# Kernel optimization log

Measured on AMD Instinct MI355X. Metric: run time of the kernel, lower is better.

Reference implementation:

```python
import jax, jax.numpy as jnp
import numpy as np

LAMBD = 0.2   # model.lambd
T_MAX = 1000  # model.T
TOL = 1e-10


def _softshrink(v, lam):
    return jnp.sign(v) * jnp.maximum(jnp.abs(v) - lam, 0.0)


def setup_inputs() -> dict:
    key = jax.random.key(0)
    k1, k2, k3 = jax.random.split(key, 3)
    n, m, N = 64, 256, 1024
    D = jax.random.normal(k1, (n, m), dtype=jnp.float32)
    D = D / jnp.linalg.norm(D, axis=0)                      # unit-norm atoms
    w = jax.random.normal(k2, (m,), dtype=jnp.float32)
    w = w / jnp.linalg.norm(w)
    x = jax.random.normal(k3, (N, n), dtype=jnp.float32)
    x = x / jnp.linalg.norm(x, axis=1, keepdims=True)       # unit-norm samples (as in generate_data)
    return {"x": x, "D": D, "w": w}


def _encode(x_t, D, lambd):
    # x_t: (n, N), D: (n, m). Faithful to encode(): ISTA with detached D/x,
    # then per-sample least-squares refinement on the support (vectorized as
    # a masked batched solve instead of a python loop over samples).
    m = D.shape[1]
    Dg = jax.lax.stop_gradient(D)
    xg = jax.lax.stop_gradient(x_t)
    # eta = 1/||D||_2^2 is a constant in torch (computed from numpy at init)
    eta = jax.lax.stop_gradient(1.0 / jnp.linalg.norm(Dg, ord=2) ** 2)
    thr = lambd * eta

    z0 = _softshrink(eta * (Dg.T @ xg), thr)                # (m, N)

    def cond(c):
        i, _, diff = c
        return (i < T_MAX) & (diff >= TOL)

    def body(c):
        i, z, _ = c
        res = Dg @ z - xg                                   # (n, N)
        znew = _softshrink(z - eta * (Dg.T @ res), thr)     # (m, N)
        return (i + 1, znew, jnp.linalg.norm(znew - z))

    _, z, _ = jax.lax.while_loop(
        cond, body, (jnp.int32(0), z0, jnp.array(jnp.inf, dtype=x_t.dtype))
    )
    z = jax.lax.stop_gradient(z)                            # ISTA output is fully detached in torch

    # Support refinement: alfa[S,i] = inv(D_S^T D_S) (D_S^T x_i - lambd*signs_S)
    mask = z != 0                                           # (m, N) support sets
    signs = jnp.sign(z)                                     # constant (sign has zero grad)
    M = mask.T.astype(x_t.dtype)                            # (N, m)
    G = D.T @ D                                             # (m, m) Gram (with grad, model.D)
    b = M * (x_t.T @ D - lambd * signs.T)                   # (N, m), zero off-support
    # Masked Gram: identity on off-support rows/cols -> block solve equals submatrix solve
    A = M[:, :, None] * M[:, None, :] * G[None] \
        + jnp.eye(m, dtype=x_t.dtype) * (1.0 - M)[:, :, None]   # (N, m, m)
    solved = jnp.linalg.solve(A, b[..., None])[..., 0]      # (N, m)
    alfa = jnp.where(mask, solved.T, z)                     # (m, N)
    return alfa


def reference(x, D, w):
    # x: (N, n). forward(): z = encode(x); y = w @ z; pred = [y, -y]
    z = _encode(x.T, D, LAMBD)                              # (m, N)
    y = w @ z                                               # (N,)
    return jnp.stack([y, -y], axis=1)                       # (N, 2)
```

## Files before the change

### kernel.cpp

```cpp
#include <hip/hip_runtime.h>

#define LAMBD 0.2f
#define KMAX 128
#define KS 64
#define OS 1.9f

using half8 = __attribute__((ext_vector_type(8))) _Float16;
using f32x4 = __attribute__((ext_vector_type(4))) float;

__device__ __forceinline__ float sshrink(float v, float thr) {
    float c = fminf(fmaxf(v, -thr), thr);
    return v - c;
}

__device__ __forceinline__ unsigned pack2(_Float16 a, _Float16 b) {
    unsigned short ua = __builtin_bit_cast(unsigned short, a);
    unsigned short ub = __builtin_bit_cast(unsigned short, b);
    return (unsigned)ua | ((unsigned)ub << 16);
}

__global__ __launch_bounds__(256) void prep_all(const float* __restrict__ xg,
                                                const float* __restrict__ Dg,
                                                float* __restrict__ ws,
                                                float* __restrict__ Gfull,
                                                float* __restrict__ cbuf)
{
    const int t = threadIdx.x;
    if (blockIdx.x == 0) {
        __shared__ __align__(16) float Dc[256 * 68];
        __shared__ __align__(16) float Bm[64 * 68];
        __shared__ float vv[64];
        __shared__ float part[4 * 64];
        __shared__ float lamsh;

        for (int i = 0; i < 64; ++i)
            Dc[t * 68 + i] = Dg[i * 256 + t];
        __syncthreads();

        const int ti = t >> 4, tj = t & 15;
        float acc[4][4];
        #pragma unroll
        for (int r = 0; r < 4; ++r)
            #pragma unroll
            for (int c = 0; c < 4; ++c) acc[r][c] = 0.f;
        for (int mm = 0; mm < 256; ++mm) {
            const float4 A = *(const float4*)&Dc[mm * 68 + 4 * ti];
            const float4 Bv = *(const float4*)&Dc[mm * 68 + 4 * tj];
            const float Ae[4] = {A.x, A.y, A.z, A.w};
            const float Be[4] = {Bv.x, Bv.y, Bv.z, Bv.w};
            #pragma unroll
            for (int r = 0; r < 4; ++r)
                #pragma unroll
                for (int c = 0; c < 4; ++c)
                    acc[r][c] += Ae[r] * Be[c];
        }
        #pragma unroll
        for (int r = 0; r < 4; ++r)
            #pragma unroll
            for (int c = 0; c < 4; ++c)
                Bm[(4 * ti + r) * 68 + (4 * tj + c)] = acc[r][c];
        if (t < 64) vv[t] = 0.125f;
        __syncthreads();

        for (int itp = 0; itp < 64; ++itp) {
            const int p = t >> 6, i = t & 63;
            float partial = 0.f;
            #pragma unroll
            for (int jj = 0; jj < 16; ++jj) {
                const int j = p * 16 + jj;
                partial += Bm[j * 68 + i] * vv[j];
            }
            part[p * 64 + i] = partial;
            __syncthreads();
            if (t < 64) {
                float nv = part[t] + part[64 + t] + part[128 + t] + part[192 + t];
                float n2 = nv * nv;
                for (int d = 1; d < 64; d <<= 1) n2 += __shfl_xor(n2, d);
                vv[t] = nv * rsqrtf(n2);
                if (t == 0) lamsh = n2;
            }
            __syncthreads();
        }
        if (t == 0) ws[0] = OS / sqrtf(lamsh);
    } else {
        __shared__ float xsh[4][64];
        const int r = blockIdx.x - 1;
        const int s0 = r * 4;
        xsh[t >> 6][t & 63] = xg[s0 * 64 + t];
        __syncthreads();

        float accG = 0.f, a0 = 0.f, a1 = 0.f, a2 = 0.f, a3 = 0.f;
        #pragma unroll
        for (int i = 0; i < 64; ++i) {
            const float dv = Dg[i * 256 + t];
            const float dr = Dg[i * 256 + r];
            accG += dr * dv;
            a0 += xsh[0][i] * dv;
            a1 += xsh[1][i] * dv;
            a2 += xsh[2][i] * dv;
            a3 += xsh[3][i] * dv;
        }
        Gfull[r * 256 + t] = accG;
        cbuf[(s0 + 0) * 256 + t] = a0;
        cbuf[(s0 + 1) * 256 + t] = a1;
        cbuf[(s0 + 2) * 256 + t] = a2;
        cbuf[(s0 + 3) * 256 + t] = a3;
    }
}

__global__ __launch_bounds__(256, 1) void ista_solve(const float* __restrict__ cbuf,
                                                     const float* __restrict__ Gfull,
                                                     const float* __restrict__ ws,
                                                     const float* __restrict__ wg,
                                                     float* __restrict__ zbuf,
                                                     int* __restrict__ kflag,
                                                     float* __restrict__ out)
{
    __shared__ __align__(16) _Float16 dbuf[2][16][264];
    __shared__ int chgs[4];
    __shared__ __align__(16) float znb[4][264];
    __shared__ __align__(16) float Gm[4][KS * (KS + 1)];
    __shared__ int   idxs[4][KS];
    __shared__ float sgns[4][KS];

    const int t = threadIdx.x;
    const int w = t >> 6, l = t & 63;
    const int n = l & 15, kg = l >> 4;
    const int s0 = blockIdx.x * 4;
    const float s = ws[0];
    const float thr = LAMBD * s;
    const float S = 1.0f / 2048.0f;
    const float FLUSH = 6.2e-5f;

    half8 wh[4][8], wl[4][8];
    #pragma unroll
    for (int a = 0; a < 4; ++a) {
        const int row = 64 * w + 16 * a + n;
        #pragma unroll
        for (int kt = 0; kt < 8; ++kt) {
            const float4 g0 = *(const float4*)&Gfull[row * 256 + kt * 32 + kg * 8];
            const float4 g1 = *(const float4*)&Gfull[row * 256 + kt * 32 + kg * 8 + 4];
            const float ge[8] = {g0.x, g0.y, g0.z, g0.w, g1.x, g1.y, g1.z, g1.w};
            half8 h, lo;
            #pragma unroll
            for (int j = 0; j < 8; ++j) {
                const int col = kt * 32 + kg * 8 + j;
                const float wv = (row == col ? 1.0f : 0.0f) - s * ge[j];
                const _Float16 whj = (_Float16)wv;
                h[j] = whj;
                lo[j] = (_Float16)((wv - (float)whj) * 2048.0f);
            }
            wh[a][kt] = h;
            wl[a][kt] = lo;
        }
    }

    float bv[4][4], z[4][4], znv[4][4];
    #pragma unroll
    for (int a = 0; a < 4; ++a)
        #pragma unroll
        for (int jj = 0; jj < 4; ++jj) {
            const int row = 64 * w + 16 * a + 4 * kg + jj;
            bv[a][jj] = (n < 4) ? s * cbuf[(s0 + n) * 256 + row] : 0.f;
            z[a][jj] = 0.f;
        }

    f32x4 acc1[4], acc2[4];
    #pragma unroll
    for (int a = 0; a < 4; ++a) {
        acc1[a] = (f32x4){0.f, 0.f, 0.f, 0.f};
        acc2[a] = (f32x4){0.f, 0.f, 0.f, 0.f};
    }

    int cur = 0;
    for (int it = 0; ; ++it) {
        bool anyflag = false;
        _Float16 dh16[4][4];
        #pragma unroll
        for (int a = 0; a < 4; ++a)
            #pragma unroll
            for (int jj = 0; jj < 4; ++jj) {
                const float P = acc1[a][jj] + S * acc2[a][jj];
                const float zn = sshrink(P + bv[a][jj], thr);
                znv[a][jj] = zn;
                const float d = zn - z[a][jj];
                const bool live = fabsf(d) >= FLUSH;
                anyflag |= live;
                const _Float16 hd = live ? (_Float16)d : (_Float16)0.0f;
                dh16[a][jj] = hd;
                z[a][jj] += (float)hd;
            }
        if (it == 1000) break;

        const int anyw = __any(anyflag);
        if (l == 0) chgs[w] = anyw;
        #pragma unroll
        for (int a = 0; a < 4; ++a) {
            const unsigned lo = pack2(dh16[a][0], dh16[a][1]);
            const unsigned hi = pack2(dh16[a][2], dh16[a][3]);
            *(uint2*)&dbuf[cur][n][64 * w + 16 * a + 4 * kg] = make_uint2(lo, hi);
        }
        __syncthreads();
        if (!(chgs[0] | chgs[1] | chgs[2] | chgs[3])) break;

        half8 dh[8];
        #pragma unroll
        for (int kt = 0; kt < 8; ++kt)
            dh[kt] = *(const half8*)&dbuf[cur][n][kt * 32 + kg * 8];

        #pragma unroll
        for (int kt = 0; kt < 8; ++kt)
            #pragma unroll
            for (int a = 0; a < 4; ++a) {
                acc1[a] = __builtin_amdgcn_mfma_f32_16x16x32_f16(wh[a][kt], dh[kt], acc1[a], 0, 0, 0);
                acc2[a] = __builtin_amdgcn_mfma_f32_16x16x32_f16(wl[a][kt], dh[kt], acc2[a], 0, 0, 0);
            }
        cur ^= 1;
    }

    if (n < 4) {
        #pragma unroll
        for (int a = 0; a < 4; ++a) {
            float4 v = make_float4(znv[a][0], znv[a][1], znv[a][2], znv[a][3]);
            *(float4*)&znb[n][64 * w + 16 * a + 4 * kg] = v;
        }
    }
    __syncthreads();

    const int sample = s0 + w;
    const float4 zz = *(const float4*)&znb[w][4 * l];
    const int c0 = zz.x != 0.f, c1 = zz.y != 0.f, c2 = zz.z != 0.f, c3 = zz.w != 0.f;
    const int cnt = c0 + c1 + c2 + c3;
    int scan = cnt;
    for (int d = 1; d < 64; d <<= 1) {
        const int v = __shfl_up(scan, d);
        if (l >= d) scan += v;
    }
    int o = scan - cnt;
    const int k = __shfl(scan, 63);

    if (k == 0) {
        if (l == 0) {
            kflag[sample] = 0;
            out[sample * 2] = 0.f;
            out[sample * 2 + 1] = 0.f;
        }
        return;
    }
    if (k > KS) {
        if (l == 0) kflag[sample] = 1;
        #pragma unroll
        for (int q = 0; q < 4; ++q)
            zbuf[sample * 256 + 4 * l + q] = ((const float*)&zz)[q];
        return;
    }
    if (l == 0) kflag[sample] = 0;

    if (c0) { idxs[w][o] = 4 * l + 0; sgns[w][o] = zz.x > 0.f ? 1.f : -1.f; ++o; }
    if (c1) { idxs[w][o] = 4 * l + 1; sgns[w][o] = zz.y > 0.f ? 1.f : -1.f; ++o; }
    if (c2) { idxs[w][o] = 4 * l + 2; sgns[w][o] = zz.z > 0.f ? 1.f : -1.f; ++o; }
    if (c3) { idxs[w][o] = 4 * l + 3; sgns[w][o] = zz.w > 0.f ? 1.f : -1.f; ++o; }

    const int   ib = idxs[w][(l < k) ? l : (k - 1)];
    const float sg = (l < k) ? sgns[w][l] : 0.f;
    float rhs = (l < k) ? (cbuf[sample * 256 + ib] - LAMBD * sg) : 0.f;

    for (int a = 0; a < k; ++a) {
        const int ra = __shfl(ib, a);
        if (l < k) Gm[w][a * (KS + 1) + l] = Gfull[ra * 256 + ib];
    }

    float dinv = 0.f;
    for (int j = 0; j < k; ++j) {
        const float Gjj = Gm[w][j * (KS + 1) + j];
        const float Ljj = sqrtf(fmaxf(Gjj, 1e-30f));
        const float iv = 1.0f / Ljj;
        float Laj = 0.f;
        if (l == j) { Gm[w][j * (KS + 1) + j] = Ljj; dinv = iv; }
        if (l > j && l < k) { Laj = Gm[w][l * (KS + 1) + j] * iv; Gm[w][l * (KS + 1) + j] = Laj; }
        for (int b = j + 1; b < k; ++b) {
            const float Lbj = Gm[w][b * (KS + 1) + j];
            if (l >= b && l < k) Gm[w][l * (KS + 1) + b] -= Laj * Lbj;
        }
    }

    float y = rhs;
    for (int j = 0; j < k; ++j) {
        const float Laj = Gm[w][l * (KS + 1) + j];
        const float yjf = __shfl(y, j) * __shfl(dinv, j);
        if (l == j) y = yjf;
        if (l > j) y -= Laj * yjf;
    }
    float xv = y;
    for (int j = k - 1; j >= 0; --j) {
        const float Lja = Gm[w][j * (KS + 1) + l];
        const float xjf = __shfl(xv, j) * __shfl(dinv, j);
        if (l == j) xv = xjf;
        if (l < j) xv -= Lja * xjf;
    }

    float acc = (l < k) ? wg[ib] * xv : 0.f;
    for (int d = 1; d < 64; d <<= 1) acc += __shfl_xor(acc, d);
    if (l == 0) { out[sample * 2] = acc; out[sample * 2 + 1] = -acc; }
}

__global__ __launch_bounds__(64) void solve_big(const float* __restrict__ Gfull,
                                                const float* __restrict__ cbuf,
                                                const float* __restrict__ wg,
                                                const float* __restrict__ zbuf,
                                                const int* __restrict__ kflag,
                                                float* __restrict__ out)
{
    __shared__ __align__(16) float Gm[KMAX * (KMAX + 1)];
    __shared__ int   idx[KMAX];
    __shared__ float sgn[KMAX];
    __shared__ float rhs[KMAX];
    __shared__ float sol[KMAX];

    const int l = threadIdx.x;
    const int sample = blockIdx.x;
    if (!kflag[sample]) return;

    const float4 zz = ((const float4*)(zbuf + sample * 256))[l];
    const int c0 = zz.x != 0.f, c1 = zz.y != 0.f, c2 = zz.z != 0.f, c3 = zz.w != 0.f;
    const int cnt = c0 + c1 + c2 + c3;
    int scan = cnt;
    for (int d = 1; d < 64; d <<= 1) {
        const int v = __shfl_up(scan, d);
        if (l >= d) scan += v;
    }
    int o = scan - cnt;
    int k = __shfl(scan, 63);
    if (k > KMAX) k = KMAX;
    if (c0) { if (o < KMAX) { idx[o] = 4 * l + 0; sgn[o] = zz.x > 0.f ? 1.f : -1.f; } ++o; }
    if (c1) { if (o < KMAX) { idx[o] = 4 * l + 1; sgn[o] = zz.y > 0.f ? 1.f : -1.f; } ++o; }
    if (c2) { if (o < KMAX) { idx[o] = 4 * l + 2; sgn[o] = zz.z > 0.f ? 1.f : -1.f; } ++o; }
    if (c3) { if (o < KMAX) { idx[o] = 4 * l + 3; sgn[o] = zz.w > 0.f ? 1.f : -1.f; } ++o; }
    __syncthreads();

    for (int a = 0; a < k; ++a) {
        const int ra = idx[a];
        for (int b = l; b < k; b += 64)
            Gm[a * (KMAX + 1) + b] = Gfull[ra * 256 + idx[b]];
    }
    for (int a = l; a < k; a += 64)
        rhs[a] = cbuf[sample * 256 + idx[a]] - LAMBD * sgn[a];
    __syncthreads();

    for (int j = 0; j < k; ++j) {
        const float Ljj = sqrtf(fmaxf(Gm[j * (KMAX + 1) + j], 1e-30f));
        const float inv = 1.0f / Ljj;
        if (l == 0) Gm[j * (KMAX + 1) + j] = Ljj;
        for (int a = j + 1 + l; a < k; a += 64)
            Gm[a * (KMAX + 1) + j] *= inv;
        __syncthreads();
        for (int b = j + 1; b < k; ++b) {
            const float Lbj = Gm[b * (KMAX + 1) + j];
            for (int a = b + l; a < k; a += 64)
                Gm[a * (KMAX + 1) + b] -= Gm[a * (KMAX + 1) + j] * Lbj;
        }
        __syncthreads();
    }
    for (int j = 0; j < k; ++j) {
        const float yj = rhs[j] / Gm[j * (KMAX + 1) + j];
        if (l == 0) sol[j] = yj;
        for (int a = j + 1 + l; a < k; a += 64)
            rhs[a] -= Gm[a * (KMAX + 1) + j] * yj;
        __syncthreads();
    }
    for (int j = k - 1; j >= 0; --j) {
        const float xj = sol[j] / Gm[j * (KMAX + 1) + j];
        if (l == 0) sol[j] = xj;
        for (int a = l; a < j; a += 64)
            sol[a] -= Gm[j * (KMAX + 1) + a] * xj;
        __syncthreads();
    }
    float acc = 0.f;
    for (int a = l; a < k; a += 64)
        acc += wg[idx[a]] * sol[a];
    for (int d = 1; d < 64; d <<= 1) acc += __shfl_xor(acc, d);
    if (l == 0) { out[sample * 2] = acc; out[sample * 2 + 1] = -acc; }
}

extern "C" void kernel_launch(void* const* d_in, const int* in_sizes, int n_in,
                              void* d_out, int out_size, void* d_ws, size_t ws_size,
                              hipStream_t stream) {
    const float* x = (const float*)d_in[0];
    const float* D = (const float*)d_in[1];
    const float* w = (const float*)d_in[2];
    float* out = (float*)d_out;
    float* ws  = (float*)d_ws;

    float* Gfull = ws + 256;
    float* zbuf  = ws + 256 + 65536;
    float* cbuf  = ws + 256 + 65536 + 262144;
    int*   kflag = (int*)(ws + 256 + 65536 + 262144 + 262144);

    prep_all<<<257, 256, 0, stream>>>(x, D, ws, Gfull, cbuf);
    ista_solve<<<256, 256, 0, stream>>>(cbuf, Gfull, ws, w, zbuf, kflag, out);
    solve_big<<<1024, 64, 0, stream>>>(Gfull, cbuf, w, zbuf, kflag, out);
}
```

Baseline: 243.7 us.

## Switch ISTA to FISTA momentum and fold large-support solve into main kernel

Replaces the over-relaxed ISTA step (1.9/L) with standard 1/L FISTA, adding Nesterov momentum on the iterate and sending deltas of the extrapolated point through the MFMA update. The aim is to reach the convergence tolerance in fewer iterations. The separate solve_big kernel and its zbuf/kflag round trip are removed: supports larger than 64 are now solved inside ista_solve by the whole block, which saves one launch but serializes these solves per block. The power iteration count also drops from 64 to 40. FISTA is not monotone, so it may converge to a different support, and the stop test on small deltas behaves differently under momentum.

```diff
diff --git a/kernel.cpp b/kernel.cpp
--- a/kernel.cpp
+++ b/kernel.cpp
@@ -3,7 +3,6 @@
 #define LAMBD 0.2f
 #define KMAX 128
 #define KS 64
-#define OS 1.9f
 
 using half8 = __attribute__((ext_vector_type(8))) _Float16;
 using f32x4 = __attribute__((ext_vector_type(4))) float;
@@ -62,7 +61,7 @@
         if (t < 64) vv[t] = 0.125f;
         __syncthreads();
 
-        for (int itp = 0; itp < 64; ++itp) {
+        for (int itp = 0; itp < 40; ++itp) {
             const int p = t >> 6, i = t & 63;
             float partial = 0.f;
             #pragma unroll
@@ -81,7 +80,7 @@
             }
             __syncthreads();
         }
-        if (t == 0) ws[0] = OS / sqrtf(lamsh);
+        if (t == 0) ws[0] = 1.0f / sqrtf(lamsh);
     } else {
         __shared__ float xsh[4][64];
         const int r = blockIdx.x - 1;
@@ -112,16 +111,18 @@
                                                      const float* __restrict__ Gfull,
                                                      const float* __restrict__ ws,
                                                      const float* __restrict__ wg,
-                                                     float* __restrict__ zbuf,
-                                                     int* __restrict__ kflag,
                                                      float* __restrict__ out)
 {
     __shared__ __align__(16) _Float16 dbuf[2][16][264];
     __shared__ int chgs[4];
     __shared__ __align__(16) float znb[4][264];
-    __shared__ __align__(16) float Gm[4][KS * (KS + 1)];
-    __shared__ int   idxs[4][KS];
-    __shared__ float sgns[4][KS];
+    __shared__ __align__(16) float GmPool[16640];
+    __shared__ int   idxPool[256];
+    __shared__ float sgnPool[256];
+    __shared__ float rhsF[KMAX];
+    __shared__ float solF[KMAX];
+    __shared__ int   big4[4];
+    __shared__ int   kbig;
 
     const int t = threadIdx.x;
     const int w = t >> 6, l = t & 63;
@@ -155,14 +156,15 @@
         }
     }
 
-    float bv[4][4], z[4][4], znv[4][4];
+    float bv[4][4], y[4][4], zo[4][4], zn[4][4];
     #pragma unroll
     for (int a = 0; a < 4; ++a)
         #pragma unroll
         for (int jj = 0; jj < 4; ++jj) {
             const int row = 64 * w + 16 * a + 4 * kg + jj;
             bv[a][jj] = (n < 4) ? s * cbuf[(s0 + n) * 256 + row] : 0.f;
-            z[a][jj] = 0.f;
+            y[a][jj] = 0.f;
+            zo[a][jj] = 0.f;
         }
 
     f32x4 acc1[4], acc2[4];
@@ -172,8 +174,11 @@
         acc2[a] = (f32x4){0.f, 0.f, 0.f, 0.f};
     }
 
+    float tk = 1.0f;
     int cur = 0;
     for (int it = 0; ; ++it) {
+        const float tk1 = 0.5f * (1.0f + sqrtf(1.0f + 4.0f * tk * tk));
+        const float beta = (tk - 1.0f) / tk1;
         bool anyflag = false;
         _Float16 dh16[4][4];
         #pragma unroll
@@ -181,15 +186,18 @@
             #pragma unroll
             for (int jj = 0; jj < 4; ++jj) {
                 const float P = acc1[a][jj] + S * acc2[a][jj];
-                const float zn = sshrink(P + bv[a][jj], thr);
-                znv[a][jj] = zn;
-                const float d = zn - z[a][jj];
+                const float z = sshrink(P + bv[a][jj], thr);
+                zn[a][jj] = z;
+                const float yn = z + beta * (z - zo[a][jj]);
+                zo[a][jj] = z;
+                const float d = yn - y[a][jj];
                 const bool live = fabsf(d) >= FLUSH;
                 anyflag |= live;
                 const _Float16 hd = live ? (_Float16)d : (_Float16)0.0f;
                 dh16[a][jj] = hd;
-                z[a][jj] += (float)hd;
-            }
+                y[a][jj] += (float)hd;
+            }
+        tk = tk1;
         if (it == 1000) break;
 
         const int anyw = __any(anyflag);
@@ -221,13 +229,17 @@
     if (n < 4) {
         #pragma unroll
         for (int a = 0; a < 4; ++a) {
-            float4 v = make_float4(znv[a][0], znv[a][1], znv[a][2], znv[a][3]);
+            float4 v = make_float4(zn[a][0], zn[a][1], zn[a][2], zn[a][3]);
             *(float4*)&znb[n][64 * w + 16 * a + 4 * kg] = v;
         }
     }
     __syncthreads();
 
     const int sample = s0 + w;
+    float* Gw = GmPool + w * (KS * (KS + 1));
+    int*   idxW = idxPool + w * KS;
+    float* sgnW = sgnPool + w * KS;
+
     const float4 zz = *(const float4*)&znb[w][4 * l];
     const int c0 = zz.x != 0.f, c1 = zz.y != 0.f, c2 = zz.z != 0.f, c3 = zz.w != 0.f;
     const int cnt = c0 + c1 + c2 + c3;
@@ -238,148 +250,140 @@
     }
     int o = scan - cnt;
     const int k = __shfl(scan, 63);
+    if (l == 0) big4[w] = (k > KS) ? 1 : 0;
 
     if (k == 0) {
-        if (l == 0) {
-            kflag[sample] = 0;
-            out[sample * 2] = 0.f;
-            out[sample * 2 + 1] = 0.f;
-        }
-        return;
-    }
-    if (k > KS) {
-        if (l == 0) kflag[sample] = 1;
-        #pragma unroll
-        for (int q = 0; q < 4; ++q)
-            zbuf[sample * 256 + 4 * l + q] = ((const float*)&zz)[q];
-        return;
-    }
-    if (l == 0) kflag[sample] = 0;
-
-    if (c0) { idxs[w][o] = 4 * l + 0; sgns[w][o] = zz.x > 0.f ? 1.f : -1.f; ++o; }
-    if (c1) { idxs[w][o] = 4 * l + 1; sgns[w][o] = zz.y > 0.f ? 1.f : -1.f; ++o; }
-    if (c2) { idxs[w][o] = 4 * l + 2; sgns[w][o] = zz.z > 0.f ? 1.f : -1.f; ++o; }
-    if (c3) { idxs[w][o] = 4 * l + 3; sgns[w][o] = zz.w > 0.f ? 1.f : -1.f; ++o; }
-
-    const int   ib = idxs[w][(l < k) ? l : (k - 1)];
-    const float sg = (l < k) ? sgns[w][l] : 0.f;
-    float rhs = (l < k) ? (cbuf[sample * 256 + ib] - LAMBD * sg) : 0.f;
-
-    for (int a = 0; a < k; ++a) {
-        const int ra = __shfl(ib, a);
-        if (l < k) Gm[w][a * (KS + 1) + l] = Gfull[ra * 256 + ib];
-    }
-
-    float dinv = 0.f;
-    for (int j = 0; j < k; ++j) {
-        const float Gjj = Gm[w][j * (KS + 1) + j];
-        const float Ljj = sqrtf(fmaxf(Gjj, 1e-30f));
-        const float iv = 1.0f / Ljj;
-        float Laj = 0.f;
-        if (l == j) { Gm[w][j * (KS + 1) + j] = Ljj; dinv = iv; }
-        if (l > j && l < k) { Laj = Gm[w][l * (KS + 1) + j] * iv; Gm[w][l * (KS + 1) + j] = Laj; }
-        for (int b = j + 1; b < k; ++b) {
-            const float Lbj = Gm[w][b * (KS + 1) + j];
-            if (l >= b && l < k) Gm[w][l * (KS + 1) + b] -= Laj * Lbj;
-        }
-    }
-
-    float y = rhs;
-    for (int j = 0; j < k; ++j) {
-        const float Laj = Gm[w][l * (KS + 1) + j];
-        const float yjf = __shfl(y, j) * __shfl(dinv, j);
-        if (l == j) y = yjf;
-        if (l > j) y -= Laj * yjf;
-    }
-    float xv = y;
-    for (int j = k - 1; j >= 0; --j) {
-        const float Lja = Gm[w][j * (KS + 1) + l];
-        const float xjf = __shfl(xv, j) * __shfl(dinv, j);
-        if (l == j) xv = xjf;
-        if (l < j) xv -= Lja * xjf;
-    }
-
-    float acc = (l < k) ? wg[ib] * xv : 0.f;
-    for (int d = 1; d < 64; d <<= 1) acc += __shfl_xor(acc, d);
-    if (l == 0) { out[sample * 2] = acc; out[sample * 2 + 1] = -acc; }
-}
-
-__global__ __launch_bounds__(64) void solve_big(const float* __restrict__ Gfull,
-                                                const float* __restrict__ cbuf,
-                                                const float* __restrict__ wg,
-                                                const float* __restrict__ zbuf,
-                                                const int* __restrict__ kflag,
-                                                float* __restrict__ out)
-{
-    __shared__ __align__(16) float Gm[KMAX * (KMAX + 1)];
-    __shared__ int   idx[KMAX];
-    __shared__ float sgn[KMAX];
-    __shared__ float rhs[KMAX];
-    __shared__ float sol[KMAX];
-
-    const int l = threadIdx.x;
-    const int sample = blockIdx.x;
-    if (!kflag[sample]) return;
-
-    const float4 zz = ((const float4*)(zbuf + sample * 256))[l];
-    const int c0 = zz.x != 0.f, c1 = zz.y != 0.f, c2 = zz.z != 0.f, c3 = zz.w != 0.f;
-    const int cnt = c0 + c1 + c2 + c3;
-    int scan = cnt;
-    for (int d = 1; d < 64; d <<= 1) {
-        const int v = __shfl_up(scan, d);
-        if (l >= d) scan += v;
-    }
-    int o = scan - cnt;
-    int k = __shfl(scan, 63);
-    if (k > KMAX) k = KMAX;
-    if (c0) { if (o < KMAX) { idx[o] = 4 * l + 0; sgn[o] = zz.x > 0.f ? 1.f : -1.f; } ++o; }
-    if (c1) { if (o < KMAX) { idx[o] = 4 * l + 1; sgn[o] = zz.y > 0.f ? 1.f : -1.f; } ++o; }
-    if (c2) { if (o < KMAX) { idx[o] = 4 * l + 2; sgn[o] = zz.z > 0.f ? 1.f : -1.f; } ++o; }
-    if (c3) { if (o < KMAX) { idx[o] = 4 * l + 3; sgn[o] = zz.w > 0.f ? 1.f : -1.f; } ++o; }
+        if (l == 0) { out[sample * 2] = 0.f; out[sample * 2 + 1] = 0.f; }
+    } else if (k <= KS) {
+        if (c0) { idxW[o] = 4 * l + 0; sgnW[o] = zz.x > 0.f ? 1.f : -1.f; ++o; }
+        if (c1) { idxW[o] = 4 * l + 1; sgnW[o] = zz.y > 0.f ? 1.f : -1.f; ++o; }
+        if (c2) { idxW[o] = 4 * l + 2; sgnW[o] = zz.z > 0.f ? 1.f : -1.f; ++o; }
+        if (c3) { idxW[o] = 4 * l + 3; sgnW[o] = zz.w > 0.f ? 1.f : -1.f; ++o; }
+        __builtin_amdgcn_wave_barrier();
+
+        const int   ib = idxW[(l < k) ? l : (k - 1)];
+        const float sg = (l < k) ? sgnW[l] : 0.f;
+        float rhs = (l < k) ? (cbuf[sample * 256 + ib] - LAMBD * sg) : 0.f;
+
+        for (int a = 0; a < k; ++a) {
+            const int ra = __shfl(ib, a);
+            if (l < k) Gw[a * (KS + 1) + l] = Gfull[ra * 256 + ib];
+        }
+        __builtin_amdgcn_wave_barrier();
+
+        float dinv = 0.f;
+        for (int j = 0; j < k; ++j) {
+            const float Gjj = Gw[j * (KS + 1) + j];
+            const float Ljj = sqrtf(fmaxf(Gjj, 1e-30f));
+            const float iv = 1.0f / Ljj;
+            float Laj = 0.f;
+            if (l == j) { Gw[j * (KS + 1) + j] = Ljj; dinv = iv; }
+            if (l > j && l < k) { Laj = Gw[l * (KS + 1) + j] * iv; Gw[l * (KS + 1) + j] = Laj; }
+            __builtin_amdgcn_wave_barrier();
+            for (int b = j + 1; b < k; ++b) {
+                const float Lbj = Gw[b * (KS + 1) + j];
+                if (l >= b && l < k) Gw[l * (KS + 1) + b] -= Laj * Lbj;
+            }
+            __builtin_amdgcn_wave_barrier();
+        }
+
+        float yv = rhs;
+        for (int j = 0; j < k; ++j) {
+            const float Laj = Gw[l * (KS + 1) + j];
+            const float yjf = __shfl(yv, j) * __shfl(dinv, j);
+            if (l == j) yv = yjf;
+            if (l > j) yv -= Laj * yjf;
+        }
+        float xv = yv;
+        for (int j = k - 1; j >= 0; --j) {
+            const float Lja = Gw[j * (KS + 1) + l];
+            const float xjf = __shfl(xv, j) * __shfl(dinv, j);
+            if (l == j) xv = xjf;
+            if (l < j) xv -= Lja * xjf;
+        }
+
+        float acc = (l < k) ? wg[ib] * xv : 0.f;
+        for (int d = 1; d < 64; d <<= 1) acc += __shfl_xor(acc, d);
+        if (l == 0) { out[sample * 2] = acc; out[sample * 2 + 1] = -acc; }
+    }
     __syncthreads();
 
-    for (int a = 0; a < k; ++a) {
-        const int ra = idx[a];
-        for (int b = l; b < k; b += 64)
-            Gm[a * (KMAX + 1) + b] = Gfull[ra * 256 + idx[b]];
-    }
-    for (int a = l; a < k; a += 64)
-        rhs[a] = cbuf[sample * 256 + idx[a]] - LAMBD * sgn[a];
-    __syncthreads();
-
-    for (int j = 0; j < k; ++j) {
-        const float Ljj = sqrtf(fmaxf(Gm[j * (KMAX + 1) + j], 1e-30f));
-        const float inv = 1.0f / Ljj;
-        if (l == 0) Gm[j * (KMAX + 1) + j] = Ljj;
-        for (int a = j + 1 + l; a < k; a += 64)
-            Gm[a * (KMAX + 1) + j] *= inv;
-        __syncthreads();
-        for (int b = j + 1; b < k; ++b) {
-            const float Lbj = Gm[b * (KMAX + 1) + j];
-            for (int a = b + l; a < k; a += 64)
-                Gm[a * (KMAX + 1) + b] -= Gm[a * (KMAX + 1) + j] * Lbj;
-        }
-        __syncthreads();
-    }
-    for (int j = 0; j < k; ++j) {
-        const float yj = rhs[j] / Gm[j * (KMAX + 1) + j];
-        if (l == 0) sol[j] = yj;
-        for (int a = j + 1 + l; a < k; a += 64)
-            rhs[a] -= Gm[a * (KMAX + 1) + j] * yj;
-        __syncthreads();
-    }
-    for (int j = k - 1; j >= 0; --j) {
-        const float xj = sol[j] / Gm[j * (KMAX + 1) + j];
-        if (l == 0) sol[j] = xj;
-        for (int a = l; a < j; a += 64)
-            sol[a] -= Gm[j * (KMAX + 1) + a] * xj;
-        __syncthreads();
-    }
-    float acc = 0.f;
-    for (int a = l; a < k; a += 64)
-        acc += wg[idx[a]] * sol[a];
-    for (int d = 1; d < 64; d <<= 1) acc += __shfl_xor(acc, d);
-    if (l == 0) { out[sample * 2] = acc; out[sample * 2 + 1] = -acc; }
+    for (int sw = 0; sw < 4; ++sw) {
+        if (!big4[sw]) continue;
+        const int smp = s0 + sw;
+        if (w == 0) {
+            const float4 z2 = *(const float4*)&znb[sw][4 * l];
+            const int d0 = z2.x != 0.f, d1 = z2.y != 0.f, d2 = z2.z != 0.f, d3 = z2.w != 0.f;
+            const int cn = d0 + d1 + d2 + d3;
+            int sc = cn;
+            for (int d = 1; d < 64; d <<= 1) {
+                const int v = __shfl_up(sc, d);
+                if (l >= d) sc += v;
+            }
+            int oo = sc - cn;
+            int kk = __shfl(sc, 63);
+            if (kk > KMAX) kk = KMAX;
+            if (l == 0) kbig = kk;
+            if (d0) { if (oo < KMAX) { idxPool[oo] = 4 * l + 0; sgnPool[oo] = z2.x > 0.f ? 1.f : -1.f; } ++oo; }
+            if (d1) { if (oo < KMAX) { idxPool[oo] = 4 * l + 1; sgnPool[oo] = z2.y > 0.f ? 1.f : -1.f; } ++oo; }
+            if (d2) { if (oo < KMAX) { idxPool[oo] = 4 * l + 2; sgnPool[oo] = z2.z > 0.f ? 1.f : -1.f; } ++oo; }
+            if (d3) { if (oo < KMAX) { idxPool[oo] = 4 * l + 3; sgnPool[oo] = z2.w > 0.f ? 1.f : -1.f; } ++oo; }
+        }
+        __syncthreads();
+        const int kk = kbig;
+        float* Gb = GmPool;
+
+        for (int a = 0; a < kk; ++a) {
+            const int ra = idxPool[a];
+            for (int b = t; b < kk; b += 256)
+                Gb[a * (KMAX + 1) + b] = Gfull[ra * 256 + idxPool[b]];
+        }
+        for (int a = t; a < kk; a += 256)
+            rhsF[a] = cbuf[smp * 256 + idxPool[a]] - LAMBD * sgnPool[a];
+        __syncthreads();
+
+        for (int j = 0; j < kk; ++j) {
+            const float Ljj = sqrtf(fmaxf(Gb[j * (KMAX + 1) + j], 1e-30f));
+            const float inv = 1.0f / Ljj;
+            if (t == 0) Gb[j * (KMAX + 1) + j] = Ljj;
+            for (int a = j + 1 + t; a < kk; a += 256)
+                Gb[a * (KMAX + 1) + j] *= inv;
+            __syncthreads();
+            for (int b = j + 1; b < kk; ++b) {
+                const float Lbj = Gb[b * (KMAX + 1) + j];
+                const int a = b + t;
+                if (a < kk) Gb[a * (KMAX + 1) + b] -= Gb[a * (KMAX + 1) + j] * Lbj;
+            }
+            __syncthreads();
+        }
+        for (int j = 0; j < kk; ++j) {
+            const float yj = rhsF[j] / Gb[j * (KMAX + 1) + j];
+            if (t == 0) solF[j] = yj;
+            for (int a = j + 1 + t; a < kk; a += 256)
+                rhsF[a] -= Gb[a * (KMAX + 1) + j] * yj;
+            __syncthreads();
+        }
+        for (int j = kk - 1; j >= 0; --j) {
+            const float xj = solF[j] / Gb[j * (KMAX + 1) + j];
+            if (t == 0) solF[j] = xj;
+            for (int a = t; a < j; a += 256)
+                solF[a] -= Gb[j * (KMAX + 1) + a] * xj;
+            __syncthreads();
+        }
+        float acc = 0.f;
+        for (int a = t; a < kk; a += 256)
+            acc += wg[idxPool[a]] * solF[a];
+        for (int d = 1; d < 64; d <<= 1) acc += __shfl_xor(acc, d);
+        if (l == 0) atomicAdd(&solF[0], 0.f);
+        if (l == 0) rhsF[64 + w] = acc;
+        __syncthreads();
+        if (t == 0) {
+            const float tot = rhsF[64] + rhsF[65] + rhsF[66] + rhsF[67];
+            out[smp * 2] = tot;
+            out[smp * 2 + 1] = -tot;
+        }
+        __syncthreads();
+    }
 }
 
 extern "C" void kernel_launch(void* const* d_in, const int* in_sizes, int n_in,
@@ -392,11 +396,8 @@
     float* ws  = (float*)d_ws;
 
     float* Gfull = ws + 256;
-    float* zbuf  = ws + 256 + 65536;
-    float* cbuf  = ws + 256 + 65536 + 262144;
-    int*   kflag = (int*)(ws + 256 + 65536 + 262144 + 262144);
+    float* cbuf  = ws + 256 + 65536;
 
     prep_all<<<257, 256, 0, stream>>>(x, D, ws, Gfull, cbuf);
-    ista_solve<<<256, 256, 0, stream>>>(cbuf, Gfull, ws, w, zbuf, kflag, out);
-    solve_big<<<1024, 64, 0, stream>>>(Gfull, cbuf, w, zbuf, kflag, out);
+    ista_solve<<<256, 256, 0, stream>>>(cbuf, Gfull, ws, w, out);
 }
```

New measurement: 237.5 us. 1.03x faster.
